# Performance work log

Hardware: AMD Instinct MI355X
Metric: run time of the kernel (lower is better)

Reference implementation:

```python
import jax, jax.numpy as jnp
import numpy as np

B, T, S = 256, 32, 128
I, H, O = 256, 1024, 256


def setup_inputs() -> dict:
    key = jax.random.key(0)
    ks = jax.random.split(key, 8)
    sc = 0.02
    return {
        "shifted_target": jax.random.normal(ks[0], (B, T, I), jnp.float32),
        "encoder_outputs": jax.random.normal(ks[1], (B, S, H), jnp.float32),
        "W_ih": jax.random.normal(ks[2], (4 * H, I), jnp.float32) * sc,
        "W_hh": jax.random.normal(ks[3], (4 * H, H), jnp.float32) * sc,
        "b_ih": jax.random.normal(ks[4], (4 * H,), jnp.float32) * sc,
        "b_hh": jax.random.normal(ks[5], (4 * H,), jnp.float32) * sc,
        "W_fc": jax.random.normal(ks[6], (O, 2 * H), jnp.float32) * sc,
        "b_fc": jax.random.normal(ks[7], (O,), jnp.float32) * sc,
    }


def reference(shifted_target, encoder_outputs, W_ih, W_hh, b_ih, b_hh, W_fc, b_fc):
    bs, tgt_len, inp = shifted_target.shape
    hid = encoder_outputs.shape[-1]
    # torch code feeds zeros (not shifted_target[:,0]) at t=0, with zero init state
    xs = shifted_target.at[:, 0, :].set(0.0)
    xs = jnp.swapaxes(xs, 0, 1)  # [T, B, I]

    def step(carry, x_t):
        h, c = carry
        gates = x_t @ W_ih.T + b_ih + h @ W_hh.T + b_hh  # [B, 4H]
        i, f, g, o = jnp.split(gates, 4, axis=-1)
        i = jax.nn.sigmoid(i)
        f = jax.nn.sigmoid(f)
        g = jnp.tanh(g)
        o = jax.nn.sigmoid(o)
        c = f * c + i * g
        h = o * jnp.tanh(c)
        # dot-product attention against encoder states
        score = jnp.einsum('bh,bsh->bs', h, encoder_outputs)
        prob = jax.nn.softmax(score, axis=-1)
        ctx = jnp.einsum('bs,bsh->bh', prob, encoder_outputs)
        out_t = jnp.concatenate([ctx, h], axis=-1) @ W_fc.T + b_fc
        return (h, c), (out_t, prob)

    h0 = jnp.zeros((bs, hid), shifted_target.dtype)
    c0 = jnp.zeros((bs, hid), shifted_target.dtype)
    _, (outs, probs) = jax.lax.scan(step, (h0, c0), xs)
    return jnp.swapaxes(outs, 0, 1), jnp.swapaxes(probs, 0, 1)
```

## Files before the change

### kernel.cpp

```cpp
#include <hip/hip_runtime.h>
#include <math.h>

#define B_  256
#define T_  32
#define S_  128
#define I_  256
#define H_  1024
#define O_  256
#define G4  4096
#define K2  2048

typedef __attribute__((ext_vector_type(8))) short bf16x8;
typedef __attribute__((ext_vector_type(4))) float f32x4;

#define MFMA16(a, b, c) __builtin_amdgcn_mfma_f32_16x16x32_bf16(a, b, c, 0, 0, 0)

__device__ __forceinline__ unsigned short f2bf(float f) {
    unsigned int u = __float_as_uint(f);
    u = (u + 0x7FFFu + ((u >> 16) & 1u)) >> 16;
    return (unsigned short)u;
}
__device__ __forceinline__ float sigm(float x) { return 1.0f / (1.0f + __expf(-x)); }

__global__ void prep_kernel(
    const float* __restrict__ x, const float* __restrict__ enc,
    const float* __restrict__ Wih, const float* __restrict__ Whh,
    const float* __restrict__ bih, const float* __restrict__ bhh,
    const float* __restrict__ Wfc,
    unsigned short* __restrict__ WihR, unsigned short* __restrict__ WhhR,
    unsigned short* __restrict__ WfcR, float* __restrict__ biasR,
    unsigned short* __restrict__ xs, unsigned short* __restrict__ encB,
    unsigned short* __restrict__ h0, unsigned short* __restrict__ h1,
    float* __restrict__ c)
{
    const long NWHH = (long)G4 * H_;
    const long NWIH = (long)G4 * I_;
    const long NWFC = (long)O_ * K2;
    const long NB   = G4;
    const long NX   = (long)B_ * T_ * I_;
    const long NE   = (long)B_ * S_ * H_;
    const long NH   = (long)B_ * H_;
    const long total = NWHH + NWIH + NWFC + NB + NX + NE + 3 * NH;
    for (long i = (long)blockIdx.x * blockDim.x + threadIdx.x; i < total;
         i += (long)gridDim.x * blockDim.x) {
        long j = i;
        if (j < NE) { encB[j] = f2bf(enc[j]); continue; }
        j -= NE;
        if (j < NWHH) {
            int r = (int)(j >> 10), k = (int)(j & 1023);
            int n = ((r & 1023) << 2) | (r >> 10);
            WhhR[(long)n * H_ + k] = f2bf(Whh[j]);
            continue;
        }
        j -= NWHH;
        if (j < NWIH) {
            int r = (int)(j >> 8), k = (int)(j & 255);
            int n = ((r & 1023) << 2) | (r >> 10);
            WihR[(long)n * I_ + k] = f2bf(Wih[j]);
            continue;
        }
        j -= NWIH;
        if (j < NWFC) { WfcR[j] = f2bf(Wfc[j]); continue; }
        j -= NWFC;
        if (j < NB) {
            int r = (int)j;
            int n = ((r & 1023) << 2) | (r >> 10);
            biasR[n] = bih[r] + bhh[r];
            continue;
        }
        j -= NB;
        if (j < NX) {
            int t = (int)((j >> 8) & 31);
            xs[j] = (t == 0) ? (unsigned short)0 : f2bf(x[j]);
            continue;
        }
        j -= NX;
        if (j < NH) { h0[j] = 0; continue; }
        j -= NH;
        if (j < NH) { h1[j] = 0; continue; }
        j -= NH;
        c[j] = 0.0f;
    }
}

__global__ __launch_bounds__(256) void step_kernel(
    const unsigned short* __restrict__ xs,
    const unsigned short* __restrict__ WihR,
    const unsigned short* __restrict__ WhhR,
    const float* __restrict__ biasR,
    const unsigned short* __restrict__ hprev,
    unsigned short* __restrict__ hnext,
    float* __restrict__ c,
    unsigned short* __restrict__ hall,
    int t)
{
    __shared__ float Gs[64 * 68];

    const int tid = threadIdx.x;
    const int lane = tid & 63, wave = tid >> 6;
    const int wm = wave >> 1, wn = wave & 1;
    const int quad = lane >> 4, l16 = lane & 15;
    const int n0 = blockIdx.x * 64, m0 = blockIdx.y * 64;

    const int ar0 = m0 + wm * 32 + l16, ar1 = ar0 + 16;
    const int br0 = n0 + wn * 32 + l16, br1 = br0 + 16;

    const unsigned short* ax0 = xs + ((long)ar0 * T_ + t) * I_ + quad * 8;
    const unsigned short* ax1 = xs + ((long)ar1 * T_ + t) * I_ + quad * 8;
    const unsigned short* ah0 = hprev + (long)ar0 * H_ + quad * 8;
    const unsigned short* ah1 = hprev + (long)ar1 * H_ + quad * 8;
    const unsigned short* bx0 = WihR + (long)br0 * I_ + quad * 8;
    const unsigned short* bx1 = WihR + (long)br1 * I_ + quad * 8;
    const unsigned short* bh0 = WhhR + (long)br0 * H_ + quad * 8;
    const unsigned short* bh1 = WhhR + (long)br1 * H_ + quad * 8;

    const f32x4 z = {0.f, 0.f, 0.f, 0.f};
    f32x4 acc00 = z, acc01 = z, acc10 = z, acc11 = z;

#pragma unroll
    for (int k0 = 0; k0 < I_; k0 += 32) {
        bf16x8 a0 = *(const bf16x8*)(ax0 + k0);
        bf16x8 a1 = *(const bf16x8*)(ax1 + k0);
        bf16x8 b0 = *(const bf16x8*)(bx0 + k0);
        bf16x8 b1 = *(const bf16x8*)(bx1 + k0);
        acc00 = MFMA16(a0, b0, acc00);
        acc01 = MFMA16(a0, b1, acc01);
        acc10 = MFMA16(a1, b0, acc10);
        acc11 = MFMA16(a1, b1, acc11);
    }
#pragma unroll 4
    for (int k0 = 0; k0 < H_; k0 += 32) {
        bf16x8 a0 = *(const bf16x8*)(ah0 + k0);
        bf16x8 a1 = *(const bf16x8*)(ah1 + k0);
        bf16x8 b0 = *(const bf16x8*)(bh0 + k0);
        bf16x8 b1 = *(const bf16x8*)(bh1 + k0);
        acc00 = MFMA16(a0, b0, acc00);
        acc01 = MFMA16(a0, b1, acc01);
        acc10 = MFMA16(a1, b0, acc10);
        acc11 = MFMA16(a1, b1, acc11);
    }

    const float bj0 = biasR[n0 + wn * 32 + l16];
    const float bj1 = biasR[n0 + wn * 32 + 16 + l16];
#pragma unroll
    for (int r = 0; r < 4; r++) {
        int row0 = wm * 32 + quad * 4 + r;
        int col0 = wn * 32 + l16;
        Gs[row0 * 68 + col0]            = acc00[r] + bj0;
        Gs[row0 * 68 + col0 + 16]       = acc01[r] + bj1;
        Gs[(row0 + 16) * 68 + col0]      = acc10[r] + bj0;
        Gs[(row0 + 16) * 68 + col0 + 16] = acc11[r] + bj1;
    }
    __syncthreads();

#pragma unroll
    for (int p = tid; p < 1024; p += 256) {
        int row = p >> 4, u = p & 15;
        float gi = Gs[row * 68 + u * 4 + 0];
        float gf = Gs[row * 68 + u * 4 + 1];
        float gg = Gs[row * 68 + u * 4 + 2];
        float go = Gs[row * 68 + u * 4 + 3];
        int b = m0 + row;
        int jg = (n0 >> 2) + u;
        float ii = sigm(gi), ff = sigm(gf), g3 = tanhf(gg), oo = sigm(go);
        float cn = ff * c[(long)b * H_ + jg] + ii * g3;
        float hh = oo * tanhf(cn);
        c[(long)b * H_ + jg] = cn;
        unsigned short hb = f2bf(hh);
        hnext[(long)b * H_ + jg] = hb;
        hall[((long)b * T_ + t) * H_ + jg] = hb;
    }
}

__global__ __launch_bounds__(256) void scores_kernel(
    const unsigned short* __restrict__ hall,
    const unsigned short* __restrict__ encB,
    float* __restrict__ probs,
    unsigned short* __restrict__ PB)
{
    __shared__ float Sc[32 * 132];

    const int tid = threadIdx.x;
    const int lane = tid & 63, wave = tid >> 6;
    const int quad = lane >> 4, l16 = lane & 15;
    const int b = blockIdx.x;
    const int nw = wave;

    const unsigned short* pa0 = hall + ((long)b * T_ + l16) * H_ + quad * 8;
    const unsigned short* pa1 = hall + ((long)b * T_ + 16 + l16) * H_ + quad * 8;
    const unsigned short* pb0 = encB + ((long)b * S_ + nw * 32 + l16) * H_ + quad * 8;
    const unsigned short* pb1 = pb0 + 16 * H_;

    const f32x4 z = {0.f, 0.f, 0.f, 0.f};
    f32x4 acc00 = z, acc01 = z, acc10 = z, acc11 = z;

#pragma unroll 4
    for (int k0 = 0; k0 < H_; k0 += 32) {
        bf16x8 a0 = *(const bf16x8*)(pa0 + k0);
        bf16x8 a1 = *(const bf16x8*)(pa1 + k0);
        bf16x8 b0 = *(const bf16x8*)(pb0 + k0);
        bf16x8 b1 = *(const bf16x8*)(pb1 + k0);
        acc00 = MFMA16(a0, b0, acc00);
        acc01 = MFMA16(a0, b1, acc01);
        acc10 = MFMA16(a1, b0, acc10);
        acc11 = MFMA16(a1, b1, acc11);
    }
#pragma unroll
    for (int r = 0; r < 4; r++) {
        int row0 = quad * 4 + r;
        int col0 = nw * 32 + l16;
        Sc[row0 * 132 + col0]            = acc00[r];
        Sc[row0 * 132 + col0 + 16]       = acc01[r];
        Sc[(row0 + 16) * 132 + col0]      = acc10[r];
        Sc[(row0 + 16) * 132 + col0 + 16] = acc11[r];
    }
    __syncthreads();
    for (int r = 0; r < 8; r++) {
        int row = wave * 8 + r;
        float v0 = Sc[row * 132 + lane];
        float v1 = Sc[row * 132 + 64 + lane];
        float mx = fmaxf(v0, v1);
#pragma unroll
        for (int off = 32; off > 0; off >>= 1) mx = fmaxf(mx, __shfl_xor(mx, off));
        float e0 = __expf(v0 - mx), e1 = __expf(v1 - mx);
        float s = e0 + e1;
#pragma unroll
        for (int off = 32; off > 0; off >>= 1) s += __shfl_xor(s, off);
        float inv = 1.0f / s;
        float p0 = e0 * inv, p1 = e1 * inv;
        long o = ((long)b * T_ + row) * S_;
        probs[o + lane] = p0;
        probs[o + 64 + lane] = p1;
        PB[o + lane] = f2bf(p0);
        PB[o + 64 + lane] = f2bf(p1);
    }
}

__global__ __launch_bounds__(256) void ctx_kernel(
    const unsigned short* __restrict__ encB,
    const unsigned short* __restrict__ PB,
    unsigned short* __restrict__ ctxo)
{
    __shared__ unsigned short Es[S_ * 256];

    const int tid = threadIdx.x;
    const int lane = tid & 63, wave = tid >> 6;
    const int quad = lane >> 4, l16 = lane & 15;
    const int b = blockIdx.x;
    const int h0 = blockIdx.y * 256;

    for (int i = tid; i < S_ * 32; i += 256) {
        int s = i >> 5, hc = (i & 31) * 8;
        *(uint4*)(Es + s * 256 + hc) =
            *(const uint4*)(encB + ((long)b * S_ + s) * H_ + h0 + hc);
    }
    bf16x8 a[2][4];
#pragma unroll
    for (int i = 0; i < 2; i++)
#pragma unroll
        for (int ks = 0; ks < 4; ks++)
            a[i][ks] = *(const bf16x8*)(PB + ((long)b * T_ + i * 16 + l16) * S_ +
                                        ks * 32 + quad * 8);
    __syncthreads();

    f32x4 acc[2][4];
    const f32x4 z = {0.f, 0.f, 0.f, 0.f};
#pragma unroll
    for (int i = 0; i < 2; i++)
#pragma unroll
        for (int j = 0; j < 4; j++) acc[i][j] = z;

    const int cw = wave * 64;
#pragma unroll
    for (int ks = 0; ks < 4; ks++) {
        const int kb = ks * 32 + quad * 8;
#pragma unroll
        for (int j = 0; j < 4; j++) {
            const int col = cw + j * 16 + l16;
            bf16x8 bb;
#pragma unroll
            for (int e = 0; e < 8; e++) bb[e] = (short)Es[(kb + e) * 256 + col];
            acc[0][j] = MFMA16(a[0][ks], bb, acc[0][j]);
            acc[1][j] = MFMA16(a[1][ks], bb, acc[1][j]);
        }
    }
#pragma unroll
    for (int i = 0; i < 2; i++)
#pragma unroll
        for (int j = 0; j < 4; j++)
#pragma unroll
            for (int r = 0; r < 4; r++) {
                int row = i * 16 + quad * 4 + r;
                int col = h0 + cw + j * 16 + l16;
                ctxo[((long)b * T_ + row) * H_ + col] = f2bf(acc[i][j][r]);
            }
}

__global__ __launch_bounds__(256) void fc_kernel(
    const unsigned short* __restrict__ ctxo,
    const unsigned short* __restrict__ hall,
    const unsigned short* __restrict__ WfcR,
    const float* __restrict__ bfc,
    float* __restrict__ out)
{
    __shared__ __align__(16) unsigned short As[64 * 40];
    __shared__ __align__(16) unsigned short Bs[128 * 40];

    const int tid = threadIdx.x;
    const int lane = tid & 63, wave = tid >> 6;
    const int wm = wave >> 1, wn = wave & 1;
    const int quad = lane >> 4, l16 = lane & 15;
    const int n0 = blockIdx.x * 128, m0 = blockIdx.y * 64;

    const int arow = tid >> 2, akc = (tid & 3) * 8;
    const int brow = tid >> 1, bkc = (tid & 1) * 16;

    f32x4 acc[2][4];
    const f32x4 z = {0.f, 0.f, 0.f, 0.f};
#pragma unroll
    for (int i = 0; i < 2; i++)
#pragma unroll
        for (int j = 0; j < 4; j++) acc[i][j] = z;

    for (int k0 = 0; k0 < K2; k0 += 32) {
        const unsigned short* asrc = (k0 < H_)
            ? ctxo + (long)(m0 + arow) * H_ + k0 + akc
            : hall + (long)(m0 + arow) * H_ + (k0 - H_) + akc;
        *(uint4*)(As + arow * 40 + akc) = *(const uint4*)asrc;
        const unsigned short* src = WfcR + (long)(n0 + brow) * K2 + k0 + bkc;
        *(uint4*)(Bs + brow * 40 + bkc)     = *(const uint4*)src;
        *(uint4*)(Bs + brow * 40 + bkc + 8) = *(const uint4*)(src + 8);
        __syncthreads();
        bf16x8 a0 = *(const bf16x8*)(As + (wm * 32 + l16) * 40 + quad * 8);
        bf16x8 a1 = *(const bf16x8*)(As + (wm * 32 + 16 + l16) * 40 + quad * 8);
#pragma unroll
        for (int j = 0; j < 4; j++) {
            bf16x8 bb = *(const bf16x8*)(Bs + (wn * 64 + j * 16 + l16) * 40 + quad * 8);
            acc[0][j] = MFMA16(a0, bb, acc[0][j]);
            acc[1][j] = MFMA16(a1, bb, acc[1][j]);
        }
        __syncthreads();
    }
#pragma unroll
    for (int i = 0; i < 2; i++)
#pragma unroll
        for (int j = 0; j < 4; j++)
#pragma unroll
            for (int r = 0; r < 4; r++) {
                int row = m0 + wm * 32 + i * 16 + quad * 4 + r;
                int col = n0 + wn * 64 + j * 16 + l16;
                out[(long)row * O_ + col] = acc[i][j][r] + bfc[col];
            }
}

extern "C" void kernel_launch(void* const* d_in, const int* in_sizes, int n_in,
                              void* d_out, int out_size, void* d_ws, size_t ws_size,
                              hipStream_t stream) {
    const float* x   = (const float*)d_in[0];
    const float* enc = (const float*)d_in[1];
    const float* Wih = (const float*)d_in[2];
    const float* Whh = (const float*)d_in[3];
    const float* bih = (const float*)d_in[4];
    const float* bhh = (const float*)d_in[5];
    const float* Wfc = (const float*)d_in[6];
    const float* bfc = (const float*)d_in[7];
    float* out = (float*)d_out;

    char* ws = (char*)d_ws;
    unsigned short* WIHR = (unsigned short*)(ws + 0);
    unsigned short* WHHR = (unsigned short*)(ws + 2097152);
    unsigned short* WFCR = (unsigned short*)(ws + 10485760);
    float*          BIAS = (float*)         (ws + 11534336);
    unsigned short* XS   = (unsigned short*)(ws + 11550720);
    unsigned short* H0   = (unsigned short*)(ws + 15745024);
    unsigned short* H1   = (unsigned short*)(ws + 16269312);
    float*          C    = (float*)         (ws + 16793600);
    unsigned short* HALL = (unsigned short*)(ws + 17842176);
    unsigned short* ENCB = (unsigned short*)(ws + 34619392);
    unsigned short* PB   = (unsigned short*)(ws + 101728256);
    unsigned short* CTX  = (unsigned short*)(ws + 103825408);

    prep_kernel<<<8192, 256, 0, stream>>>(x, enc, Wih, Whh, bih, bhh, Wfc,
                                          WIHR, WHHR, WFCR, BIAS, XS, ENCB,
                                          H0, H1, C);

    for (int t = 0; t < T_; t++) {
        const unsigned short* hp = (t & 1) ? H1 : H0;
        unsigned short* hn = (t & 1) ? H0 : H1;
        step_kernel<<<dim3(64, 4), 256, 0, stream>>>(XS, WIHR, WHHR, BIAS,
                                                     hp, hn, C, HALL, t);
    }

    scores_kernel<<<B_, 256, 0, stream>>>(HALL, ENCB,
                                          out + (long)B_ * T_ * O_, PB);
    ctx_kernel<<<dim3(B_, 4), 256, 0, stream>>>(ENCB, PB, CTX);
    fc_kernel<<<dim3(2, 128), 256, 0, stream>>>(CTX, HALL, WFCR, bfc, out);
}
```

Before: 1.113 ms.

## Fuse LSTM time loop into persistent kernel with register-resident weights and grid barrier

The 32 per-timestep step launches are replaced by one persistent kernel of 256 blocks. Each block keeps its slice of W_ih/W_hh in registers, splits K across waves, reduces partial sums through shared memory, keeps the cell state in registers, and synchronises all blocks between steps with an atomic grid barrier. The prep kernel is also vectorised to convert 8 elements per thread with 16-byte stores. This removes launch overhead and repeated weight reloads at each step. In exchange it relies on all 256 blocks being co-resident and adds barrier spin cost, and the large register footprint may spill.

```diff
diff --git a/kernel.cpp b/kernel.cpp
--- a/kernel.cpp
+++ b/kernel.cpp
@@ -20,6 +20,17 @@
     u = (u + 0x7FFFu + ((u >> 16) & 1u)) >> 16;
     return (unsigned short)u;
 }
+__device__ __forceinline__ unsigned int pack2(float a, float b) {
+    return (unsigned int)f2bf(a) | ((unsigned int)f2bf(b) << 16);
+}
+__device__ __forceinline__ uint4 cvt8(const float* p) {
+    float4 f0 = *(const float4*)p;
+    float4 f1 = *(const float4*)(p + 4);
+    uint4 v;
+    v.x = pack2(f0.x, f0.y); v.y = pack2(f0.z, f0.w);
+    v.z = pack2(f1.x, f1.y); v.w = pack2(f1.z, f1.w);
+    return v;
+}
 __device__ __forceinline__ float sigm(float x) { return 1.0f / (1.0f + __expf(-x)); }
 
 __global__ void prep_kernel(
@@ -30,145 +41,198 @@
     unsigned short* __restrict__ WihR, unsigned short* __restrict__ WhhR,
     unsigned short* __restrict__ WfcR, float* __restrict__ biasR,
     unsigned short* __restrict__ xs, unsigned short* __restrict__ encB,
-    unsigned short* __restrict__ h0, unsigned short* __restrict__ h1,
-    float* __restrict__ c)
+    unsigned short* __restrict__ h0)
 {
-    const long NWHH = (long)G4 * H_;
-    const long NWIH = (long)G4 * I_;
-    const long NWFC = (long)O_ * K2;
-    const long NB   = G4;
-    const long NX   = (long)B_ * T_ * I_;
-    const long NE   = (long)B_ * S_ * H_;
-    const long NH   = (long)B_ * H_;
-    const long total = NWHH + NWIH + NWFC + NB + NX + NE + 3 * NH;
+    const long U_ENC = ((long)B_ * S_ * H_) >> 3;
+    const long U_WHH = ((long)G4 * H_) >> 3;
+    const long U_WIH = ((long)G4 * I_) >> 3;
+    const long U_WFC = ((long)O_ * K2) >> 3;
+    const long U_X   = ((long)B_ * T_ * I_) >> 3;
+    const long U_H0  = ((long)B_ * H_) >> 3;
+    const long U_B   = G4 >> 3;
+    const long total = U_ENC + U_WHH + U_WIH + U_WFC + U_X + U_H0 + U_B;
     for (long i = (long)blockIdx.x * blockDim.x + threadIdx.x; i < total;
          i += (long)gridDim.x * blockDim.x) {
         long j = i;
-        if (j < NE) { encB[j] = f2bf(enc[j]); continue; }
-        j -= NE;
-        if (j < NWHH) {
-            int r = (int)(j >> 10), k = (int)(j & 1023);
+        if (j < U_ENC) {
+            long e = j << 3;
+            *(uint4*)(encB + e) = cvt8(enc + e);
+            continue;
+        }
+        j -= U_ENC;
+        if (j < U_WHH) {
+            long e = j << 3;
+            int r = (int)(e >> 10), k = (int)(e & 1023);
             int n = ((r & 1023) << 2) | (r >> 10);
-            WhhR[(long)n * H_ + k] = f2bf(Whh[j]);
-            continue;
-        }
-        j -= NWHH;
-        if (j < NWIH) {
-            int r = (int)(j >> 8), k = (int)(j & 255);
+            *(uint4*)(WhhR + (long)n * H_ + k) = cvt8(Whh + e);
+            continue;
+        }
+        j -= U_WHH;
+        if (j < U_WIH) {
+            long e = j << 3;
+            int r = (int)(e >> 8), k = (int)(e & 255);
             int n = ((r & 1023) << 2) | (r >> 10);
-            WihR[(long)n * I_ + k] = f2bf(Wih[j]);
-            continue;
-        }
-        j -= NWIH;
-        if (j < NWFC) { WfcR[j] = f2bf(Wfc[j]); continue; }
-        j -= NWFC;
-        if (j < NB) {
-            int r = (int)j;
-            int n = ((r & 1023) << 2) | (r >> 10);
-            biasR[n] = bih[r] + bhh[r];
-            continue;
-        }
-        j -= NB;
-        if (j < NX) {
-            int t = (int)((j >> 8) & 31);
-            xs[j] = (t == 0) ? (unsigned short)0 : f2bf(x[j]);
-            continue;
-        }
-        j -= NX;
-        if (j < NH) { h0[j] = 0; continue; }
-        j -= NH;
-        if (j < NH) { h1[j] = 0; continue; }
-        j -= NH;
-        c[j] = 0.0f;
-    }
-}
-
-__global__ __launch_bounds__(256) void step_kernel(
+            *(uint4*)(WihR + (long)n * I_ + k) = cvt8(Wih + e);
+            continue;
+        }
+        j -= U_WIH;
+        if (j < U_WFC) {
+            long e = j << 3;
+            *(uint4*)(WfcR + e) = cvt8(Wfc + e);
+            continue;
+        }
+        j -= U_WFC;
+        if (j < U_X) {
+            long e = j << 3;
+            int tt = (int)((e >> 8) & 31);
+            if (tt == 0) {
+                uint4 zz = {0u, 0u, 0u, 0u};
+                *(uint4*)(xs + e) = zz;
+            } else {
+                *(uint4*)(xs + e) = cvt8(x + e);
+            }
+            continue;
+        }
+        j -= U_X;
+        if (j < U_H0) {
+            uint4 zz = {0u, 0u, 0u, 0u};
+            *(uint4*)(h0 + (j << 3)) = zz;
+            continue;
+        }
+        j -= U_H0;
+        {
+            long e = j << 3;
+#pragma unroll
+            for (int q = 0; q < 8; q++) {
+                int r = (int)e + q;
+                int n = ((r & 1023) << 2) | (r >> 10);
+                biasR[n] = bih[r] + bhh[r];
+            }
+        }
+    }
+}
+
+__global__ __launch_bounds__(256, 1) void rec_kernel(
     const unsigned short* __restrict__ xs,
     const unsigned short* __restrict__ WihR,
     const unsigned short* __restrict__ WhhR,
     const float* __restrict__ biasR,
-    const unsigned short* __restrict__ hprev,
-    unsigned short* __restrict__ hnext,
-    float* __restrict__ c,
+    unsigned short* __restrict__ h0,
+    unsigned short* __restrict__ h1,
     unsigned short* __restrict__ hall,
-    int t)
+    unsigned int* __restrict__ bar)
 {
-    __shared__ float Gs[64 * 68];
+    __shared__ float P[4][64][64];
 
     const int tid = threadIdx.x;
     const int lane = tid & 63, wave = tid >> 6;
-    const int wm = wave >> 1, wn = wave & 1;
     const int quad = lane >> 4, l16 = lane & 15;
-    const int n0 = blockIdx.x * 64, m0 = blockIdx.y * 64;
-
-    const int ar0 = m0 + wm * 32 + l16, ar1 = ar0 + 16;
-    const int br0 = n0 + wn * 32 + l16, br1 = br0 + 16;
-
-    const unsigned short* ax0 = xs + ((long)ar0 * T_ + t) * I_ + quad * 8;
-    const unsigned short* ax1 = xs + ((long)ar1 * T_ + t) * I_ + quad * 8;
-    const unsigned short* ah0 = hprev + (long)ar0 * H_ + quad * 8;
-    const unsigned short* ah1 = hprev + (long)ar1 * H_ + quad * 8;
-    const unsigned short* bx0 = WihR + (long)br0 * I_ + quad * 8;
-    const unsigned short* bx1 = WihR + (long)br1 * I_ + quad * 8;
-    const unsigned short* bh0 = WhhR + (long)br0 * H_ + quad * 8;
-    const unsigned short* bh1 = WhhR + (long)br1 * H_ + quad * 8;
-
-    const f32x4 z = {0.f, 0.f, 0.f, 0.f};
-    f32x4 acc00 = z, acc01 = z, acc10 = z, acc11 = z;
-
-#pragma unroll
-    for (int k0 = 0; k0 < I_; k0 += 32) {
-        bf16x8 a0 = *(const bf16x8*)(ax0 + k0);
-        bf16x8 a1 = *(const bf16x8*)(ax1 + k0);
-        bf16x8 b0 = *(const bf16x8*)(bx0 + k0);
-        bf16x8 b1 = *(const bf16x8*)(bx1 + k0);
-        acc00 = MFMA16(a0, b0, acc00);
-        acc01 = MFMA16(a0, b1, acc01);
-        acc10 = MFMA16(a1, b0, acc10);
-        acc11 = MFMA16(a1, b1, acc11);
-    }
-#pragma unroll 4
-    for (int k0 = 0; k0 < H_; k0 += 32) {
-        bf16x8 a0 = *(const bf16x8*)(ah0 + k0);
-        bf16x8 a1 = *(const bf16x8*)(ah1 + k0);
-        bf16x8 b0 = *(const bf16x8*)(bh0 + k0);
-        bf16x8 b1 = *(const bf16x8*)(bh1 + k0);
-        acc00 = MFMA16(a0, b0, acc00);
-        acc01 = MFMA16(a0, b1, acc01);
-        acc10 = MFMA16(a1, b0, acc10);
-        acc11 = MFMA16(a1, b1, acc11);
-    }
-
-    const float bj0 = biasR[n0 + wn * 32 + l16];
-    const float bj1 = biasR[n0 + wn * 32 + 16 + l16];
-#pragma unroll
-    for (int r = 0; r < 4; r++) {
-        int row0 = wm * 32 + quad * 4 + r;
-        int col0 = wn * 32 + l16;
-        Gs[row0 * 68 + col0]            = acc00[r] + bj0;
-        Gs[row0 * 68 + col0 + 16]       = acc01[r] + bj1;
-        Gs[(row0 + 16) * 68 + col0]      = acc10[r] + bj0;
-        Gs[(row0 + 16) * 68 + col0 + 16] = acc11[r] + bj1;
-    }
-    __syncthreads();
-
-#pragma unroll
-    for (int p = tid; p < 1024; p += 256) {
-        int row = p >> 4, u = p & 15;
-        float gi = Gs[row * 68 + u * 4 + 0];
-        float gf = Gs[row * 68 + u * 4 + 1];
-        float gg = Gs[row * 68 + u * 4 + 2];
-        float go = Gs[row * 68 + u * 4 + 3];
-        int b = m0 + row;
-        int jg = (n0 >> 2) + u;
-        float ii = sigm(gi), ff = sigm(gf), g3 = tanhf(gg), oo = sigm(go);
-        float cn = ff * c[(long)b * H_ + jg] + ii * g3;
-        float hh = oo * tanhf(cn);
-        c[(long)b * H_ + jg] = cn;
-        unsigned short hb = f2bf(hh);
-        hnext[(long)b * H_ + jg] = hb;
-        hall[((long)b * T_ + t) * H_ + jg] = hb;
+    const int bx = blockIdx.x;
+    const int n0 = (bx & 63) * 64;
+    const int m0 = (bx >> 6) * 64;
+    const int wk0 = wave * 320;
+
+    bf16x8 bfrag[4][10];
+#pragma unroll
+    for (int ni = 0; ni < 4; ni++) {
+        const long nr = n0 + ni * 16 + l16;
+#pragma unroll
+        for (int kk = 0; kk < 10; kk++) {
+            int kg = wk0 + kk * 32 + quad * 8;
+            bfrag[ni][kk] = (kg < I_)
+                ? *(const bf16x8*)(WihR + nr * I_ + kg)
+                : *(const bf16x8*)(WhhR + nr * H_ + (kg - I_));
+        }
+    }
+
+    const int erow = tid >> 2;
+    const int eu4 = (tid & 3) * 4;
+    f32x4 bias4[4];
+#pragma unroll
+    for (int uu = 0; uu < 4; uu++)
+        bias4[uu] = *(const f32x4*)(biasR + n0 + (eu4 + uu) * 4);
+    float creg[4] = {0.f, 0.f, 0.f, 0.f};
+
+    const long hwoff = (long)(m0 + erow) * H_ + (n0 >> 2) + eu4;
+
+    for (int t = 0; t < T_; t++) {
+        const unsigned short* hc = (t & 1) ? h1 : h0;
+        unsigned short* hn = (t & 1) ? h0 : h1;
+
+        f32x4 acc[4][4];
+        const f32x4 z = {0.f, 0.f, 0.f, 0.f};
+#pragma unroll
+        for (int mi = 0; mi < 4; mi++)
+#pragma unroll
+            for (int ni = 0; ni < 4; ni++) acc[mi][ni] = z;
+
+#pragma unroll
+        for (int kk = 0; kk < 10; kk++) {
+            int kg = wk0 + kk * 32 + quad * 8;
+            bf16x8 a[4];
+            if (kg < I_) {
+#pragma unroll
+                for (int mi = 0; mi < 4; mi++)
+                    a[mi] = *(const bf16x8*)(xs +
+                        ((long)(m0 + mi * 16 + l16) * T_ + t) * I_ + kg);
+            } else {
+#pragma unroll
+                for (int mi = 0; mi < 4; mi++)
+                    a[mi] = *(const bf16x8*)(hc +
+                        (long)(m0 + mi * 16 + l16) * H_ + (kg - I_));
+            }
+#pragma unroll
+            for (int ni = 0; ni < 4; ni++)
+#pragma unroll
+                for (int mi = 0; mi < 4; mi++)
+                    acc[mi][ni] = MFMA16(a[mi], bfrag[ni][kk], acc[mi][ni]);
+        }
+
+#pragma unroll
+        for (int mi = 0; mi < 4; mi++)
+#pragma unroll
+            for (int ni = 0; ni < 4; ni++)
+#pragma unroll
+                for (int r = 0; r < 4; r++)
+                    P[wave][mi * 16 + quad * 4 + r][ni * 16 + l16] = acc[mi][ni][r];
+        __syncthreads();
+
+        unsigned int hv[2];
+        {
+            unsigned short hbuf[4];
+#pragma unroll
+            for (int uu = 0; uu < 4; uu++) {
+                f32x4 g = bias4[uu];
+#pragma unroll
+                for (int w = 0; w < 4; w++) {
+                    f32x4 pv = *(const f32x4*)&P[w][erow][(eu4 + uu) * 4];
+                    g[0] += pv[0]; g[1] += pv[1]; g[2] += pv[2]; g[3] += pv[3];
+                }
+                float ii = sigm(g[0]), ff = sigm(g[1]);
+                float gg = tanhf(g[2]), oo = sigm(g[3]);
+                float cn = ff * creg[uu] + ii * gg;
+                creg[uu] = cn;
+                hbuf[uu] = f2bf(oo * tanhf(cn));
+            }
+            hv[0] = (unsigned int)hbuf[0] | ((unsigned int)hbuf[1] << 16);
+            hv[1] = (unsigned int)hbuf[2] | ((unsigned int)hbuf[3] << 16);
+        }
+        *(uint2*)(hn + hwoff) = *(uint2*)hv;
+        *(uint2*)(hall + ((long)(m0 + erow) * T_ + t) * H_ + (n0 >> 2) + eu4) =
+            *(uint2*)hv;
+
+        __threadfence();
+        __syncthreads();
+        if (tid == 0) {
+            __hip_atomic_fetch_add(bar, 1u, __ATOMIC_ACQ_REL,
+                                   __HIP_MEMORY_SCOPE_AGENT);
+            const unsigned int tgt = 256u * (unsigned int)(t + 1);
+            while (__hip_atomic_load(bar, __ATOMIC_ACQUIRE,
+                                     __HIP_MEMORY_SCOPE_AGENT) < tgt)
+                __builtin_amdgcn_s_sleep(2);
+        }
+        __syncthreads();
+        __threadfence();
     }
 }
 
@@ -374,22 +438,18 @@
     unsigned short* XS   = (unsigned short*)(ws + 11550720);
     unsigned short* H0   = (unsigned short*)(ws + 15745024);
     unsigned short* H1   = (unsigned short*)(ws + 16269312);
-    float*          C    = (float*)         (ws + 16793600);
-    unsigned short* HALL = (unsigned short*)(ws + 17842176);
-    unsigned short* ENCB = (unsigned short*)(ws + 34619392);
-    unsigned short* PB   = (unsigned short*)(ws + 101728256);
-    unsigned short* CTX  = (unsigned short*)(ws + 103825408);
-
-    prep_kernel<<<8192, 256, 0, stream>>>(x, enc, Wih, Whh, bih, bhh, Wfc,
-                                          WIHR, WHHR, WFCR, BIAS, XS, ENCB,
-                                          H0, H1, C);
-
-    for (int t = 0; t < T_; t++) {
-        const unsigned short* hp = (t & 1) ? H1 : H0;
-        unsigned short* hn = (t & 1) ? H0 : H1;
-        step_kernel<<<dim3(64, 4), 256, 0, stream>>>(XS, WIHR, WHHR, BIAS,
-                                                     hp, hn, C, HALL, t);
-    }
+    unsigned short* HALL = (unsigned short*)(ws + 16793600);
+    unsigned short* ENCB = (unsigned short*)(ws + 33570816);
+    unsigned short* PB   = (unsigned short*)(ws + 100679680);
+    unsigned short* CTX  = (unsigned short*)(ws + 102776832);
+    unsigned int*   BAR  = (unsigned int*)  (ws + 119554048);
+
+    hipMemsetAsync(BAR, 0, 256, stream);
+
+    prep_kernel<<<4096, 256, 0, stream>>>(x, enc, Wih, Whh, bih, bhh, Wfc,
+                                          WIHR, WHHR, WFCR, BIAS, XS, ENCB, H0);
+
+    rec_kernel<<<256, 256, 0, stream>>>(XS, WIHR, WHHR, BIAS, H0, H1, HALL, BAR);
 
     scores_kernel<<<B_, 256, 0, stream>>>(HALL, ENCB,
                                           out + (long)B_ * T_ * O_, PB);
```

After: 2.527 ms. 2.27x slower.
